# Optimization experiments

Hardware: AMD Instinct MI355X
Metric: run time of the kernel (lower is better)

Reference implementation:

```python
import jax, jax.numpy as jnp
import numpy as np

N_STREAMS = 4
DIM = 1024  # per-stream channels C
SINKHORN_ITERS = 50
SINKHORN_TAU = 0.1
RMS_EPS = 1.1920929e-07  # torch.finfo(float32).eps (nn.RMSNorm default eps=None)


def setup_inputs() -> dict:
    key = jax.random.key(0)
    ks = jax.random.split(key, 6)
    B, T = 4, 2048
    n, C = N_STREAMS, DIM
    wd = n * C  # widened_dim
    x = jax.random.normal(ks[0], (B, T, wd), dtype=jnp.float32)
    # projection weights, init std=0.01 (stored as [out, in] like nn.Linear)
    W_res = 0.01 * jax.random.normal(ks[1], (n * n, wd), dtype=jnp.float32)
    W_pre = 0.01 * jax.random.normal(ks[2], (n, wd), dtype=jnp.float32)
    W_post = 0.01 * jax.random.normal(ks[3], (n, wd), dtype=jnp.float32)
    # base logits
    H_res_base = jnp.full((n, n), -0.5, dtype=jnp.float32)
    H_res_base = H_res_base.at[jnp.arange(n), jnp.arange(n)].set(0.0)
    H_pre_base = jnp.zeros((n,), dtype=jnp.float32).at[0].set(1.0)
    H_post_base = jnp.zeros((n,), dtype=jnp.float32)
    gate = jnp.array([5.0], dtype=jnp.float32)
    # branch_fn stand-in: single C->C linear
    W_branch = (1.0 / np.sqrt(C)) * jax.random.normal(ks[4], (C, C), dtype=jnp.float32)
    return {"x": x, "W_res": W_res, "W_pre": W_pre, "W_post": W_post,
            "H_res_base": H_res_base, "H_pre_base": H_pre_base,
            "H_post_base": H_post_base, "gate": gate, "W_branch": W_branch}


def sinkhorn_log(logits, num_iters=SINKHORN_ITERS, tau=SINKHORN_TAU):
    # logits: [..., n, n]
    Z = logits / tau
    u0 = jnp.zeros(Z.shape[:-1], Z.dtype)  # [..., n]
    v0 = jnp.zeros_like(u0)

    def step(carry, _):
        u, v = carry
        u = -jax.nn.logsumexp(Z + v[..., None, :], axis=-1)
        v = -jax.nn.logsumexp(Z + u[..., :, None], axis=-2)
        return (u, v), None

    (u, v), _ = jax.lax.scan(step, (u0, v0), None, length=num_iters)
    return jnp.exp(Z + u[..., :, None] + v[..., None, :])


def reference(x, W_res, W_pre, W_post, H_res_base, H_pre_base, H_post_base, gate, W_branch):
    B, T, nC = x.shape
    n = N_STREAMS
    C = nC // n
    # RMSNorm (no affine)
    x_norm = x * jax.lax.rsqrt(jnp.mean(x * x, axis=-1, keepdims=True) + RMS_EPS)
    # projections (Linear stores [out, in])
    H_res_logits = (x_norm @ W_res.T).reshape(B, T, n, n) + H_res_base
    H_pre_logits = x_norm @ W_pre.T + H_pre_base
    H_post_logits = x_norm @ W_post.T + H_post_base
    H_res = sinkhorn_log(H_res_logits)
    H_pre = jax.nn.softmax(H_pre_logits, axis=-1)
    H_post = jax.nn.softmax(H_post_logits, axis=-1)
    g = jax.nn.sigmoid(gate)[0]  # eval mode: no exploration noise
    I = jnp.eye(n, dtype=H_res.dtype)
    H_res = (1.0 - g) * I + g * H_res
    x_streams = x.reshape(B, T, n, C)
    x_pre = jnp.einsum('btnc,btn->btc', x_streams, H_pre)
    y = x_pre @ W_branch  # branch_fn stand-in
    x_mixed = jnp.einsum('btij,btjc->btic', H_res, x_streams)
    y_distributed = jnp.einsum('btc,btn->btnc', y, H_post)
    return (x_mixed + y_distributed).reshape(B, T, nC)
```

## Files before the change

kernel.cpp:

```cpp
#include <hip/hip_runtime.h>
#include <cstdint>
#include <cstddef>

#define NTOK 8192
#define WD   4096
#define CD   1024
#define EPS_RMS 1.1920929e-07f
#define TAU_INV 10.0f

using half8  = __attribute__((ext_vector_type(8))) _Float16;
using half4v = __attribute__((ext_vector_type(4))) _Float16;
using f32x4  = __attribute__((ext_vector_type(4))) float;

__global__ __launch_bounds__(256) void k_prep(const float* __restrict__ W,
                                              _Float16* __restrict__ WT,
                                              const float* __restrict__ Wres,
                                              const float* __restrict__ Wpre,
                                              const float* __restrict__ Wpost,
                                              _Float16* __restrict__ Wcat) {
  if (blockIdx.x < 256) {
    __shared__ float tile[64][65];
    const int t  = threadIdx.x;
    const int c0 = (blockIdx.x & 15) * 64;
    const int k0 = (blockIdx.x >> 4) * 64;
    const int a = t & 63, b = t >> 6;
#pragma unroll
    for (int i = 0; i < 16; ++i) {
      int k = b + i * 4;
      tile[k][a] = W[(size_t)(k0 + k) * CD + (c0 + a)];
    }
    __syncthreads();
#pragma unroll
    for (int i = 0; i < 16; ++i) {
      int c = b + i * 4;
      WT[(size_t)(c0 + c) * CD + (k0 + a)] = (_Float16)tile[a][c];
    }
  } else {
    const int id  = (blockIdx.x - 256) * 256 + threadIdx.x;
    const int row = id >> 10;
    const int kq  = id & 1023;
    float4 v = make_float4(0.f, 0.f, 0.f, 0.f);
    if (row < 16)      v = *(const float4*)(Wres + (size_t)row * WD + kq * 4);
    else if (row < 20) v = *(const float4*)(Wpre + (size_t)(row - 16) * WD + kq * 4);
    else if (row < 24) v = *(const float4*)(Wpost + (size_t)(row - 20) * WD + kq * 4);
    half4v h;
    h[0] = (_Float16)v.x; h[1] = (_Float16)v.y; h[2] = (_Float16)v.z; h[3] = (_Float16)v.w;
    *(half4v*)(Wcat + (size_t)row * WD + kq * 4) = h;
  }
}

#define KCH 512
__global__ __launch_bounds__(512, 6) void k_stats4(
    const float* __restrict__ x, const _Float16* __restrict__ Wcat,
    const float* __restrict__ baseRes, const float* __restrict__ basePre,
    const float* __restrict__ basePost, const float* __restrict__ gate,
    float* __restrict__ HpostOut, float* __restrict__ HresF,
    _Float16* __restrict__ xpre)
{
  __shared__ float Lpart[8][16][32];
  __shared__ float ssPart[8][16];
  __shared__ float invS[16];
  __shared__ float HpreS[16][4];

  const int t    = threadIdx.x;
  const int lane = t & 63;
  const int p    = t >> 6;
  const int tok0 = blockIdx.x * 16;
  const int fr   = lane & 15, kg = lane >> 4;

  const float*    xr = x    + (size_t)(tok0 + fr) * WD + p * KCH + kg * 8;
  const _Float16* w0 = Wcat + (size_t)fr * WD        + p * KCH + kg * 8;
  const _Float16* w1 = Wcat + (size_t)(16 + fr) * WD + p * KCH + kg * 8;

  f32x4 acc0 = {0.f, 0.f, 0.f, 0.f};
  f32x4 acc1 = {0.f, 0.f, 0.f, 0.f};
  float ss = 0.f;

#pragma unroll
  for (int kt = 0; kt < 16; ++kt) {
    const int ko = kt * 32;
    const float4 u = *(const float4*)(xr + ko);
    const float4 v = *(const float4*)(xr + ko + 4);
    const half8 b0 = *(const half8*)(w0 + ko);
    const half8 b1 = *(const half8*)(w1 + ko);
    ss += u.x * u.x + u.y * u.y + u.z * u.z + u.w * u.w;
    ss += v.x * v.x + v.y * v.y + v.z * v.z + v.w * v.w;
    half8 a;
    a[0] = (_Float16)u.x; a[1] = (_Float16)u.y; a[2] = (_Float16)u.z; a[3] = (_Float16)u.w;
    a[4] = (_Float16)v.x; a[5] = (_Float16)v.y; a[6] = (_Float16)v.z; a[7] = (_Float16)v.w;
    acc0 = __builtin_amdgcn_mfma_f32_16x16x32_f16(a, b0, acc0, 0, 0, 0);
    acc1 = __builtin_amdgcn_mfma_f32_16x16x32_f16(a, b1, acc1, 0, 0, 0);
  }

  ss += __shfl_xor(ss, 16);
  ss += __shfl_xor(ss, 32);
  if (lane < 16) ssPart[p][lane] = ss;

#pragma unroll
  for (int r = 0; r < 4; ++r) {
    Lpart[p][kg * 4 + r][fr]      = acc0[r];
    Lpart[p][kg * 4 + r][16 + fr] = acc1[r];
  }
  __syncthreads();

  if (t < 16) {
    float s = 0.f;
#pragma unroll
    for (int pp = 0; pp < 8; ++pp) s += ssPart[pp][t];
    const float inv = rsqrtf(s * (1.0f / (float)WD) + EPS_RMS);
    invS[t] = inv;
    float pr[4], q[4];
#pragma unroll
    for (int j = 0; j < 4; ++j) {
      float lp = 0.f, lq = 0.f;
#pragma unroll
      for (int pp = 0; pp < 8; ++pp) {
        lp += Lpart[pp][t][16 + j];
        lq += Lpart[pp][t][20 + j];
      }
      pr[j] = fmaf(lp, inv, basePre[j]);
      q[j]  = fmaf(lq, inv, basePost[j]);
    }
    {
      const float m = fmaxf(fmaxf(pr[0], pr[1]), fmaxf(pr[2], pr[3]));
      float s2 = 0.f;
#pragma unroll
      for (int j = 0; j < 4; ++j) { pr[j] = __expf(pr[j] - m); s2 += pr[j]; }
      const float rs = 1.0f / s2;
#pragma unroll
      for (int j = 0; j < 4; ++j) HpreS[t][j] = pr[j] * rs;
    }
    {
      const float m = fmaxf(fmaxf(q[0], q[1]), fmaxf(q[2], q[3]));
      float s2 = 0.f;
#pragma unroll
      for (int j = 0; j < 4; ++j) { q[j] = __expf(q[j] - m); s2 += q[j]; }
      const float rs = 1.0f / s2;
      float4 qv; qv.x = q[0] * rs; qv.y = q[1] * rs; qv.z = q[2] * rs; qv.w = q[3] * rs;
      *(float4*)(HpostOut + (size_t)(tok0 + t) * 4) = qv;
    }
  }
  __syncthreads();

  if (t < 256) {
    const int tk  = t >> 4;
    const int l16 = t & 15;
    float Lsum = 0.f;
#pragma unroll
    for (int pp = 0; pp < 8; ++pp) Lsum += Lpart[pp][tk][l16];
    const float Z = fmaf(Lsum, invS[tk], baseRes[l16]) * TAU_INV;
    const int i = l16 >> 2, j = l16 & 3;
    float u = 0.0f, v = 0.0f;
    for (int itr = 0; itr < 50; ++itr) {
      float a = Z + v;
      float m = fmaxf(a, __shfl_xor(a, 1)); m = fmaxf(m, __shfl_xor(m, 2));
      float s = __expf(a - m);
      s += __shfl_xor(s, 1); s += __shfl_xor(s, 2);
      u = -(m + __logf(s));
      float b = Z + u;
      float m2 = fmaxf(b, __shfl_xor(b, 4)); m2 = fmaxf(m2, __shfl_xor(m2, 8));
      float s2 = __expf(b - m2);
      s2 += __shfl_xor(s2, 4); s2 += __shfl_xor(s2, 8);
      v = -(m2 + __logf(s2));
    }
    const float H = __expf(Z + u + v);
    const float gg = 1.0f / (1.0f + __expf(-gate[0]));
    HresF[(size_t)(tok0 + tk) * 16 + l16] = gg * H + ((i == j) ? (1.0f - gg) : 0.0f);
  } else {
    const int q16 = (t - 256) >> 4;
    const int l16 = t & 15;
    const int tok = tok0 + q16;
    const float p0 = HpreS[q16][0], p1 = HpreS[q16][1];
    const float p2 = HpreS[q16][2], p3 = HpreS[q16][3];
    const float* xrow = x + (size_t)tok * WD;
    _Float16* xp = xpre + (size_t)tok * CD;
#pragma unroll 2
    for (int it = 0; it < 16; ++it) {
      const int c4 = it * 64 + l16 * 4;
      const float4 s0 = *(const float4*)(xrow + c4);
      const float4 s1 = *(const float4*)(xrow + CD + c4);
      const float4 s2 = *(const float4*)(xrow + 2 * CD + c4);
      const float4 s3 = *(const float4*)(xrow + 3 * CD + c4);
      half4v h;
      h[0] = (_Float16)(p0 * s0.x + p1 * s1.x + p2 * s2.x + p3 * s3.x);
      h[1] = (_Float16)(p0 * s0.y + p1 * s1.y + p2 * s2.y + p3 * s3.y);
      h[2] = (_Float16)(p0 * s0.z + p1 * s1.z + p2 * s2.z + p3 * s3.z);
      h[3] = (_Float16)(p0 * s0.w + p1 * s1.w + p2 * s2.w + p3 * s3.w);
      *(half4v*)(xp + c4) = h;
    }
  }
}

#define LDK 72
#define SMEM_BYTES 38912
__global__ __launch_bounds__(256, 4) void k_gemm_epi(
    const _Float16* __restrict__ xpre, const _Float16* __restrict__ WT,
    const float* __restrict__ x, const float* __restrict__ HresF,
    const float* __restrict__ Hpost, float* __restrict__ out)
{
  __shared__ __align__(16) char smem[SMEM_BYTES];
  _Float16* As = (_Float16*)smem;
  _Float16* Bs = (_Float16*)(smem + 9216);

  const int tid  = threadIdx.x;
  const int nb   = blockIdx.x & 7;
  const int mb   = blockIdx.x >> 3;
  const int tok0 = mb * 64;
  const int cb   = nb * 128;
  const int lane = tid & 63, wid = tid >> 6;
  const int wc   = wid * 32;
  const int fr = lane & 15, kg = lane >> 4;

  const int sr = tid >> 3;
  const int sk = (tid & 7) * 8;
  const _Float16* pA = xpre + (size_t)(tok0 + sr) * CD + sk;
  const _Float16* pB = WT   + (size_t)(cb  + sr) * CD + sk;

  f32x4 acc[4][2];
#pragma unroll
  for (int m = 0; m < 4; ++m)
#pragma unroll
    for (int n = 0; n < 2; ++n) { f32x4 z = {0.f, 0.f, 0.f, 0.f}; acc[m][n] = z; }

  half8 a0 = *(const half8*)(pA);
  half8 a1 = *(const half8*)(pA + 32 * CD);
  half8 b0 = *(const half8*)(pB);
  half8 b1 = *(const half8*)(pB + 32 * CD);
  half8 b2 = *(const half8*)(pB + 64 * CD);
  half8 b3 = *(const half8*)(pB + 96 * CD);

  for (int kt = 0; kt < 16; ++kt) {
    __syncthreads();
    *(half8*)&As[sr * LDK + sk]        = a0;
    *(half8*)&As[(sr + 32) * LDK + sk] = a1;
    *(half8*)&Bs[sr * LDK + sk]        = b0;
    *(half8*)&Bs[(sr + 32) * LDK + sk] = b1;
    *(half8*)&Bs[(sr + 64) * LDK + sk] = b2;
    *(half8*)&Bs[(sr + 96) * LDK + sk] = b3;
    if (kt < 15) {
      const int ko = (kt + 1) * 64;
      a0 = *(const half8*)(pA + ko);
      a1 = *(const half8*)(pA + 32 * CD + ko);
      b0 = *(const half8*)(pB + ko);
      b1 = *(const half8*)(pB + 32 * CD + ko);
      b2 = *(const half8*)(pB + 64 * CD + ko);
      b3 = *(const half8*)(pB + 96 * CD + ko);
    }
    __syncthreads();
#pragma unroll
    for (int kk = 0; kk < 2; ++kk) {
      half8 af[4], bf[2];
#pragma unroll
      for (int m = 0; m < 4; ++m)
        af[m] = *(const half8*)&As[(m * 16 + fr) * LDK + kk * 32 + kg * 8];
#pragma unroll
      for (int n = 0; n < 2; ++n)
        bf[n] = *(const half8*)&Bs[(wc + n * 16 + fr) * LDK + kk * 32 + kg * 8];
#pragma unroll
      for (int m = 0; m < 4; ++m)
#pragma unroll
        for (int n = 0; n < 2; ++n)
          acc[m][n] = __builtin_amdgcn_mfma_f32_16x16x32_f16(af[m], bf[n], acc[m][n], 0, 0, 0);
    }
  }
  __syncthreads();

  float* yl = (float*)smem;
  float* Hs = (float*)(smem + 33792);
#pragma unroll
  for (int m = 0; m < 4; ++m)
#pragma unroll
    for (int reg = 0; reg < 4; ++reg) {
      const int tl = m * 16 + kg * 4 + reg;
#pragma unroll
      for (int n = 0; n < 2; ++n)
        yl[tl * 132 + wc + n * 16 + fr] = acc[m][n][reg];
    }
  for (int idx = tid; idx < 64 * 20; idx += 256) {
    const int tl = idx / 20, e = idx % 20;
    Hs[idx] = (e < 16) ? HresF[(size_t)(tok0 + tl) * 16 + e]
                       : Hpost[(size_t)(tok0 + tl) * 4 + (e - 16)];
  }
  __syncthreads();

#pragma unroll 2
  for (int it = 0; it < 8; ++it) {
    const int idx = it * 256 + tid;
    const int tl  = idx >> 5;
    const int cq  = (idx & 31) * 4;
    const int c   = cb + cq;
    const size_t trow = (size_t)(tok0 + tl) * WD;
    const float4 yv = *(const float4*)&yl[tl * 132 + cq];
    const float4 x0 = *(const float4*)(x + trow + c);
    const float4 x1 = *(const float4*)(x + trow + CD + c);
    const float4 x2 = *(const float4*)(x + trow + 2 * CD + c);
    const float4 x3 = *(const float4*)(x + trow + 3 * CD + c);
    const float* H = &Hs[tl * 20];
#pragma unroll
    for (int i = 0; i < 4; ++i) {
      const float h0 = H[i * 4 + 0], h1 = H[i * 4 + 1];
      const float h2 = H[i * 4 + 2], h3 = H[i * 4 + 3], hy = H[16 + i];
      float4 o;
      o.x = h0 * x0.x + h1 * x1.x + h2 * x2.x + h3 * x3.x + hy * yv.x;
      o.y = h0 * x0.y + h1 * x1.y + h2 * x2.y + h3 * x3.y + hy * yv.y;
      o.z = h0 * x0.z + h1 * x1.z + h2 * x2.z + h3 * x3.z + hy * yv.z;
      o.w = h0 * x0.w + h1 * x1.w + h2 * x2.w + h3 * x3.w + hy * yv.w;
      *(float4*)(out + trow + i * CD + c) = o;
    }
  }
}

extern "C" void kernel_launch(void* const* d_in, const int* in_sizes, int n_in,
                              void* d_out, int out_size, void* d_ws, size_t ws_size,
                              hipStream_t stream) {
  const float* x        = (const float*)d_in[0];
  const float* Wres     = (const float*)d_in[1];
  const float* Wpre     = (const float*)d_in[2];
  const float* Wpost    = (const float*)d_in[3];
  const float* baseRes  = (const float*)d_in[4];
  const float* basePre  = (const float*)d_in[5];
  const float* basePost = (const float*)d_in[6];
  const float* gate     = (const float*)d_in[7];
  const float* Wb       = (const float*)d_in[8];
  float* out = (float*)d_out;

  char* ws = (char*)d_ws;
  _Float16* xpre  = (_Float16*)(ws);
  _Float16* WT    = (_Float16*)(ws + 16777216);
  float*    HresF = (float*)(ws + 19398656);
  float*    Hpst  = (float*)(ws + 19922944);
  _Float16* Wcat  = (_Float16*)(ws + 20054016);

  k_prep<<<384, 256, 0, stream>>>(Wb, WT, Wres, Wpre, Wpost, Wcat);
  k_stats4<<<512, 512, 0, stream>>>(x, Wcat, baseRes, basePre, basePost, gate,
                                    Hpst, HresF, xpre);
  k_gemm_epi<<<1024, 256, 0, stream>>>(xpre, WT, x, HresF, Hpst, out);
}
```

Before: 146.6 us.

## Load GEMM MFMA fragments directly from global memory, dropping LDS staging

The branch GEMM in k_gemm_epi no longer stages A and B tiles through LDS with per-iteration barriers. Each wave now reads its MFMA fragments straight from global memory (relying on L1/L2 for reuse across the four waves that share the A tile), and the H coefficients are loaded into LDS before the GEMM so that load overlaps with it. This removes two __syncthreads per k-step and the LDS write/read traffic. In exchange global and L2 traffic rises, since A is re-read by every wave, the explicit register prefetch is gone, and the strided 16-byte loads may be less coalesced.

Measured after the change: 209.8 us. 43.1% more time.

```diff
diff --git a/kernel.cpp b/kernel.cpp
--- a/kernel.cpp
+++ b/kernel.cpp
@@ -191,16 +191,15 @@
   }
 }
 
-#define LDK 72
-#define SMEM_BYTES 38912
+#define SMEM_EPI 38912
 __global__ __launch_bounds__(256, 4) void k_gemm_epi(
     const _Float16* __restrict__ xpre, const _Float16* __restrict__ WT,
     const float* __restrict__ x, const float* __restrict__ HresF,
     const float* __restrict__ Hpost, float* __restrict__ out)
 {
-  __shared__ __align__(16) char smem[SMEM_BYTES];
-  _Float16* As = (_Float16*)smem;
-  _Float16* Bs = (_Float16*)(smem + 9216);
+  __shared__ __align__(16) char smem[SMEM_EPI];
+  float* yl = (float*)smem;
+  float* Hs = (float*)(smem + 33792);
 
   const int tid  = threadIdx.x;
   const int nb   = blockIdx.x & 7;
@@ -211,76 +210,54 @@
   const int wc   = wid * 32;
   const int fr = lane & 15, kg = lane >> 4;
 
-  const int sr = tid >> 3;
-  const int sk = (tid & 7) * 8;
-  const _Float16* pA = xpre + (size_t)(tok0 + sr) * CD + sk;
-  const _Float16* pB = WT   + (size_t)(cb  + sr) * CD + sk;
-
-  f32x4 acc[4][2];
-#pragma unroll
-  for (int m = 0; m < 4; ++m)
-#pragma unroll
-    for (int n = 0; n < 2; ++n) { f32x4 z = {0.f, 0.f, 0.f, 0.f}; acc[m][n] = z; }
-
-  half8 a0 = *(const half8*)(pA);
-  half8 a1 = *(const half8*)(pA + 32 * CD);
-  half8 b0 = *(const half8*)(pB);
-  half8 b1 = *(const half8*)(pB + 32 * CD);
-  half8 b2 = *(const half8*)(pB + 64 * CD);
-  half8 b3 = *(const half8*)(pB + 96 * CD);
-
-  for (int kt = 0; kt < 16; ++kt) {
-    __syncthreads();
-    *(half8*)&As[sr * LDK + sk]        = a0;
-    *(half8*)&As[(sr + 32) * LDK + sk] = a1;
-    *(half8*)&Bs[sr * LDK + sk]        = b0;
-    *(half8*)&Bs[(sr + 32) * LDK + sk] = b1;
-    *(half8*)&Bs[(sr + 64) * LDK + sk] = b2;
-    *(half8*)&Bs[(sr + 96) * LDK + sk] = b3;
-    if (kt < 15) {
-      const int ko = (kt + 1) * 64;
-      a0 = *(const half8*)(pA + ko);
-      a1 = *(const half8*)(pA + 32 * CD + ko);
-      b0 = *(const half8*)(pB + ko);
-      b1 = *(const half8*)(pB + 32 * CD + ko);
-      b2 = *(const half8*)(pB + 64 * CD + ko);
-      b3 = *(const half8*)(pB + 96 * CD + ko);
-    }
-    __syncthreads();
-#pragma unroll
-    for (int kk = 0; kk < 2; ++kk) {
-      half8 af[4], bf[2];
-#pragma unroll
-      for (int m = 0; m < 4; ++m)
-        af[m] = *(const half8*)&As[(m * 16 + fr) * LDK + kk * 32 + kg * 8];
-#pragma unroll
-      for (int n = 0; n < 2; ++n)
-        bf[n] = *(const half8*)&Bs[(wc + n * 16 + fr) * LDK + kk * 32 + kg * 8];
-#pragma unroll
-      for (int m = 0; m < 4; ++m)
-#pragma unroll
-        for (int n = 0; n < 2; ++n)
-          acc[m][n] = __builtin_amdgcn_mfma_f32_16x16x32_f16(af[m], bf[n], acc[m][n], 0, 0, 0);
-    }
-  }
-  __syncthreads();
-
-  float* yl = (float*)smem;
-  float* Hs = (float*)(smem + 33792);
-#pragma unroll
-  for (int m = 0; m < 4; ++m)
-#pragma unroll
-    for (int reg = 0; reg < 4; ++reg) {
-      const int tl = m * 16 + kg * 4 + reg;
-#pragma unroll
-      for (int n = 0; n < 2; ++n)
-        yl[tl * 132 + wc + n * 16 + fr] = acc[m][n][reg];
-    }
   for (int idx = tid; idx < 64 * 20; idx += 256) {
     const int tl = idx / 20, e = idx % 20;
     Hs[idx] = (e < 16) ? HresF[(size_t)(tok0 + tl) * 16 + e]
                        : Hpost[(size_t)(tok0 + tl) * 4 + (e - 16)];
   }
+
+  const _Float16* pA = xpre + (size_t)(tok0 + fr) * CD + kg * 8;
+  const _Float16* pB = WT   + (size_t)(cb + wc + fr) * CD + kg * 8;
+
+  f32x4 acc[4][2];
+#pragma unroll
+  for (int m = 0; m < 4; ++m)
+#pragma unroll
+    for (int n = 0; n < 2; ++n) { f32x4 z = {0.f, 0.f, 0.f, 0.f}; acc[m][n] = z; }
+
+#pragma unroll 2
+  for (int kt = 0; kt < 16; ++kt) {
+    const int ko = kt * 64;
+    half8 af[4][2], bf[2][2];
+#pragma unroll
+    for (int m = 0; m < 4; ++m) {
+      af[m][0] = *(const half8*)(pA + (size_t)m * 16 * CD + ko);
+      af[m][1] = *(const half8*)(pA + (size_t)m * 16 * CD + ko + 32);
+    }
+#pragma unroll
+    for (int n = 0; n < 2; ++n) {
+      bf[n][0] = *(const half8*)(pB + (size_t)n * 16 * CD + ko);
+      bf[n][1] = *(const half8*)(pB + (size_t)n * 16 * CD + ko + 32);
+    }
+#pragma unroll
+    for (int kk = 0; kk < 2; ++kk)
+#pragma unroll
+      for (int m = 0; m < 4; ++m)
+#pragma unroll
+        for (int n = 0; n < 2; ++n)
+          acc[m][n] = __builtin_amdgcn_mfma_f32_16x16x32_f16(af[m][kk], bf[n][kk],
+                                                             acc[m][n], 0, 0, 0);
+  }
+
+#pragma unroll
+  for (int m = 0; m < 4; ++m)
+#pragma unroll
+    for (int reg = 0; reg < 4; ++reg) {
+      const int tl = m * 16 + kg * 4 + reg;
+#pragma unroll
+      for (int n = 0; n < 2; ++n)
+        yl[tl * 132 + wc + n * 16 + fr] = acc[m][n][reg];
+    }
   __syncthreads();
 
 #pragma unroll 2
```

## Split fused GEMM+epilogue into separate GEMM and streaming epilogue kernels

Applied to the files above, without the earlier changes.

Unfuses the branch GEMM from the stream-mixing epilogue. The GEMM now writes y straight into the first C columns of each output row. A new k_epi kernel then reads y back, mixes it with x and stores all four streams using nontemporal stores. The aim is to lower GEMM LDS use and register pressure and to give the epilogue fully coalesced full-row access. The cost is an extra round trip of y through global memory plus one more kernel launch. k_epi reads y from the stream-0 slot and then overwrites that slot, so correctness relies on each thread reading its y before it stores.

New measurement: 145.1 us. Within noise of the previous version (-1.0%).

```diff
diff --git a/kernel.cpp b/kernel.cpp
--- a/kernel.cpp
+++ b/kernel.cpp
@@ -192,16 +192,12 @@
 }
 
 #define LDK 72
-#define SMEM_BYTES 38912
-__global__ __launch_bounds__(256, 4) void k_gemm_epi(
+__global__ __launch_bounds__(256, 4) void k_gemm(
     const _Float16* __restrict__ xpre, const _Float16* __restrict__ WT,
-    const float* __restrict__ x, const float* __restrict__ HresF,
-    const float* __restrict__ Hpost, float* __restrict__ out)
+    float* __restrict__ out)
 {
-  __shared__ __align__(16) char smem[SMEM_BYTES];
-  _Float16* As = (_Float16*)smem;
-  _Float16* Bs = (_Float16*)(smem + 9216);
-
+  __shared__ _Float16 As[64 * LDK];
+  __shared__ _Float16 Bs[128 * LDK];
   const int tid  = threadIdx.x;
   const int nb   = blockIdx.x & 7;
   const int mb   = blockIdx.x >> 3;
@@ -263,49 +259,48 @@
           acc[m][n] = __builtin_amdgcn_mfma_f32_16x16x32_f16(af[m], bf[n], acc[m][n], 0, 0, 0);
     }
   }
-  __syncthreads();
-
-  float* yl = (float*)smem;
-  float* Hs = (float*)(smem + 33792);
+
 #pragma unroll
   for (int m = 0; m < 4; ++m)
 #pragma unroll
     for (int reg = 0; reg < 4; ++reg) {
       const int tl = m * 16 + kg * 4 + reg;
+      float* yrow = out + (size_t)(tok0 + tl) * WD + cb + wc;
 #pragma unroll
       for (int n = 0; n < 2; ++n)
-        yl[tl * 132 + wc + n * 16 + fr] = acc[m][n][reg];
-    }
-  for (int idx = tid; idx < 64 * 20; idx += 256) {
-    const int tl = idx / 20, e = idx % 20;
-    Hs[idx] = (e < 16) ? HresF[(size_t)(tok0 + tl) * 16 + e]
-                       : Hpost[(size_t)(tok0 + tl) * 4 + (e - 16)];
+        yrow[n * 16 + fr] = acc[m][n][reg];
+    }
+}
+
+__global__ __launch_bounds__(256) void k_epi(
+    const float* __restrict__ x, const float* __restrict__ HresF,
+    const float* __restrict__ Hpost, float* out)
+{
+  __shared__ float Hs[4][20];
+  const int tid  = threadIdx.x;
+  const int tok0 = blockIdx.x * 4;
+  if (tid < 80) {
+    const int tl = tid / 20, e = tid % 20;
+    Hs[tl][e] = (e < 16) ? HresF[(size_t)(tok0 + tl) * 16 + e]
+                         : Hpost[(size_t)(tok0 + tl) * 4 + (e - 16)];
   }
   __syncthreads();
-
+  const int c4 = tid * 4;
 #pragma unroll 2
-  for (int it = 0; it < 8; ++it) {
-    const int idx = it * 256 + tid;
-    const int tl  = idx >> 5;
-    const int cq  = (idx & 31) * 4;
-    const int c   = cb + cq;
-    const size_t trow = (size_t)(tok0 + tl) * WD;
-    const float4 yv = *(const float4*)&yl[tl * 132 + cq];
-    const float4 x0 = *(const float4*)(x + trow + c);
-    const float4 x1 = *(const float4*)(x + trow + CD + c);
-    const float4 x2 = *(const float4*)(x + trow + 2 * CD + c);
-    const float4 x3 = *(const float4*)(x + trow + 3 * CD + c);
-    const float* H = &Hs[tl * 20];
-#pragma unroll
-    for (int i = 0; i < 4; ++i) {
-      const float h0 = H[i * 4 + 0], h1 = H[i * 4 + 1];
-      const float h2 = H[i * 4 + 2], h3 = H[i * 4 + 3], hy = H[16 + i];
-      float4 o;
-      o.x = h0 * x0.x + h1 * x1.x + h2 * x2.x + h3 * x3.x + hy * yv.x;
-      o.y = h0 * x0.y + h1 * x1.y + h2 * x2.y + h3 * x3.y + hy * yv.y;
-      o.z = h0 * x0.z + h1 * x1.z + h2 * x2.z + h3 * x3.z + hy * yv.z;
-      o.w = h0 * x0.w + h1 * x1.w + h2 * x2.w + h3 * x3.w + hy * yv.w;
-      *(float4*)(out + trow + i * CD + c) = o;
+  for (int tk = 0; tk < 4; ++tk) {
+    const size_t trow = (size_t)(tok0 + tk) * WD;
+    const f32x4 yv = *(const f32x4*)(out + trow + c4);
+    const f32x4 x0 = *(const f32x4*)(x + trow + c4);
+    const f32x4 x1 = *(const f32x4*)(x + trow + CD + c4);
+    const f32x4 x2 = *(const f32x4*)(x + trow + 2 * CD + c4);
+    const f32x4 x3 = *(const f32x4*)(x + trow + 3 * CD + c4);
+    const float* H = Hs[tk];
+#pragma unroll
+    for (int s = 0; s < 4; ++s) {
+      const float h0 = H[s * 4 + 0], h1 = H[s * 4 + 1];
+      const float h2 = H[s * 4 + 2], h3 = H[s * 4 + 3], hy = H[16 + s];
+      f32x4 o = h0 * x0 + h1 * x1 + h2 * x2 + h3 * x3 + hy * yv;
+      __builtin_nontemporal_store(o, (f32x4*)(out + trow + s * CD + c4));
     }
   }
 }
@@ -334,5 +329,6 @@
   k_prep<<<384, 256, 0, stream>>>(Wb, WT, Wres, Wpre, Wpost, Wcat);
   k_stats4<<<512, 512, 0, stream>>>(x, Wcat, baseRes, basePre, basePost, gate,
                                     Hpst, HresF, xpre);
-  k_gemm_epi<<<1024, 256, 0, stream>>>(xpre, WT, x, HresF, Hpst, out);
-}
+  k_gemm<<<1024, 256, 0, stream>>>(xpre, WT, out);
+  k_epi<<<2048, 256, 0, stream>>>(x, HresF, Hpst, out);
+}
```
